# Performance work log

Measured on AMD Instinct MI355X. Metric: run time of the kernel, lower is better.

Reference implementation:

```python
import jax, jax.numpy as jnp
import numpy as np

N, E, B, T = 50000, 800000, 256, 50
IN_DIM, H, C1, C2, Q_DIM, LH = 128, 4, 32, 128, 32, 128
EPS = 1e-5


def setup_inputs() -> dict:
    key = jax.random.key(0)
    ks = jax.random.split(key, 24)
    g = 0.05
    inp = {
        'x': jax.random.normal(ks[0], (N, IN_DIM), jnp.float32),
        'edge_index': jax.random.randint(ks[1], (2, E), 0, N, jnp.int32),
        'batch': jnp.sort(jax.random.randint(ks[2], (N,), 0, B, jnp.int32)),
        'quant': jax.random.normal(ks[3], (B, T, Q_DIM), jnp.float32),
        # GATConv(128 -> 32, heads=4, concat)
        'gat_W': jax.random.normal(ks[4], (IN_DIM, H * C1), jnp.float32) * g,
        'gat_att_src': jax.random.normal(ks[5], (H, C1), jnp.float32) * g,
        'gat_att_dst': jax.random.normal(ks[6], (H, C1), jnp.float32) * g,
        'gat_b': jnp.zeros((H * C1,), jnp.float32),
        # BN1 over 128 channels (eval mode)
        'bn1_gamma': jnp.ones((H * C1,), jnp.float32),
        'bn1_beta': jnp.zeros((H * C1,), jnp.float32),
        'bn1_mean': jax.random.normal(ks[7], (H * C1,), jnp.float32) * 0.01,
        'bn1_var': jnp.ones((H * C1,), jnp.float32),
        # GCNConv(128 -> 128)
        'gcn_W': jax.random.normal(ks[8], (H * C1, C2), jnp.float32) * g,
        'gcn_b': jnp.zeros((C2,), jnp.float32),
        'bn2_gamma': jnp.ones((C2,), jnp.float32),
        'bn2_beta': jnp.zeros((C2,), jnp.float32),
        'bn2_mean': jax.random.normal(ks[9], (C2,), jnp.float32) * 0.01,
        'bn2_var': jnp.ones((C2,), jnp.float32),
        # GlobalAttention gate: Linear(C2 -> 1)
        'gate_W': jax.random.normal(ks[10], (1, C2), jnp.float32) * g,
        'gate_b': jnp.zeros((1,), jnp.float32),
        # LSTM(Q_DIM -> LH), torch gate order i,f,g,o
        'lstm_Wih': jax.random.normal(ks[11], (4 * LH, Q_DIM), jnp.float32) * g,
        'lstm_Whh': jax.random.normal(ks[12], (4 * LH, LH), jnp.float32) * g,
        'lstm_bih': jnp.zeros((4 * LH,), jnp.float32),
        'lstm_bhh': jnp.zeros((4 * LH,), jnp.float32),
        # final Linear(C2+LH -> 1)
        'fc_W': jax.random.normal(ks[13], (1, C2 + LH), jnp.float32) * g,
        'fc_b': jnp.zeros((1,), jnp.float32),
    }
    return inp


def _segment_softmax(e, seg, num_segments):
    m = jax.ops.segment_max(e, seg, num_segments=num_segments)
    ex = jnp.exp(e - m[seg])
    s = jax.ops.segment_sum(ex, seg, num_segments=num_segments)
    return ex / (s[seg] + 1e-16)


def _bn_eval(x, gamma, beta, mean, var):
    return gamma * (x - mean) * jax.lax.rsqrt(var + EPS) + beta


def _forward(x, edge_index, batch, quant,
             gat_W, gat_att_src, gat_att_dst, gat_b,
             bn1_gamma, bn1_beta, bn1_mean, bn1_var,
             gcn_W, gcn_b, bn2_gamma, bn2_beta, bn2_mean, bn2_var,
             gate_W, gate_b,
             lstm_Wih, lstm_Whh, lstm_bih, lstm_bhh,
             fc_W, fc_b):
    n = x.shape[0]
    loops = jnp.arange(n, dtype=edge_index.dtype)
    ei = jnp.concatenate([edge_index, jnp.stack([loops, loops])], axis=1)  # add self loops
    src, dst = ei[0], ei[1]

    # ---- GATConv ----
    xw = (x @ gat_W).reshape(n, H, C1)                      # [N,H,C1]
    a_src = jnp.sum(xw * gat_att_src, axis=-1)              # [N,H]
    a_dst = jnp.sum(xw * gat_att_dst, axis=-1)
    e = jax.nn.leaky_relu(a_src[src] + a_dst[dst], 0.2)     # [E+N,H]
    alpha = _segment_softmax(e, dst, n)                     # softmax over in-edges per dst
    msg = xw[src] * alpha[:, :, None]                       # [E+N,H,C1]
    h = jax.ops.segment_sum(msg, dst, num_segments=n).reshape(n, H * C1) + gat_b

    h = jax.nn.elu(h)
    h = _bn_eval(h, bn1_gamma, bn1_beta, bn1_mean, bn1_var)

    # ---- GCNConv (sym-normalized with self loops) ----
    deg = jax.ops.segment_sum(jnp.ones_like(dst, jnp.float32), dst, num_segments=n)
    dinv = jnp.where(deg > 0, jax.lax.rsqrt(deg), 0.0)
    norm = dinv[src] * dinv[dst]                            # [E+N]
    hw = h @ gcn_W                                          # [N,C2]
    h2 = jax.ops.segment_sum(hw[src] * norm[:, None], dst, num_segments=n) + gcn_b

    h2 = jax.nn.elu(h2)
    h2 = _bn_eval(h2, bn2_gamma, bn2_beta, bn2_mean, bn2_var)

    # ---- GlobalAttention pooling over graphs ----
    gate = (h2 @ gate_W.T + gate_b)[:, 0]                   # [N]
    score = _segment_softmax(gate, batch, B)
    graph_rep = jax.ops.segment_sum(score[:, None] * h2, batch, num_segments=B)  # [B,C2]

    # ---- LSTM over quant series ----
    def step(carry, xt):
        hh, cc = carry
        gates = xt @ lstm_Wih.T + hh @ lstm_Whh.T + lstm_bih + lstm_bhh
        i, f, gg, o = jnp.split(gates, 4, axis=-1)
        cc = jax.nn.sigmoid(f) * cc + jax.nn.sigmoid(i) * jnp.tanh(gg)
        hh = jax.nn.sigmoid(o) * jnp.tanh(cc)
        return (hh, cc), None

    h0 = jnp.zeros((B, LH), quant.dtype)
    (hT, _), _ = jax.lax.scan(step, (h0, h0), jnp.swapaxes(quant, 0, 1))

    combined = jnp.concatenate([graph_rep, hT], axis=1)     # [B, C2+LH]
    out = (combined @ fc_W.T + fc_b)[:, 0]                  # [B]
    return out


def reference(x, edge_index, batch, quant,
              gat_W, gat_att_src, gat_att_dst, gat_b,
              bn1_gamma, bn1_beta, bn1_mean, bn1_var,
              gcn_W, gcn_b, bn2_gamma, bn2_beta, bn2_mean, bn2_var,
              gate_W, gate_b,
              lstm_Wih, lstm_Whh, lstm_bih, lstm_bhh,
              fc_W, fc_b):
    return _forward(x, edge_index, batch, quant,
                    gat_W, gat_att_src, gat_att_dst, gat_b,
                    bn1_gamma, bn1_beta, bn1_mean, bn1_var,
                    gcn_W, gcn_b, bn2_gamma, bn2_beta, bn2_mean, bn2_var,
                    gate_W, gate_b,
                    lstm_Wih, lstm_Whh, lstm_bih, lstm_bhh,
                    fc_W, fc_b)
```

## Files before the change

kernel.cpp:

```cpp
#include <hip/hip_runtime.h>
#include <cfloat>
#include <cstddef>

constexpr int KIN   = 128;
constexpr int KQD   = 32;
constexpr int KT    = 50;
constexpr int KLH   = 128;
constexpr float BN_EPS = 1e-5f;

typedef __attribute__((ext_vector_type(8))) short bf16x8;
typedef __attribute__((ext_vector_type(4))) float f32x4;
union U8 { bf16x8 v; unsigned u[4]; };

__device__ __forceinline__ float elu_f(float x)  { return x > 0.f ? x : (__expf(x) - 1.f); }
__device__ __forceinline__ float leaky_f(float x){ return x > 0.f ? x : 0.2f * x; }

__device__ __forceinline__ unsigned bfpack(float lo, float hi) {
    unsigned ul = __float_as_uint(lo), uh = __float_as_uint(hi);
    ul += 0x7FFFu + ((ul >> 16) & 1u);
    uh += 0x7FFFu + ((uh >> 16) & 1u);
    return (ul >> 16) | (uh & 0xFFFF0000u);
}
__device__ __forceinline__ unsigned short bf1(float v) {
    unsigned u = __float_as_uint(v);
    u += 0x7FFFu + ((u >> 16) & 1u);
    return (unsigned short)(u >> 16);
}
__device__ __forceinline__ float bflo(unsigned u) { return __uint_as_float(u << 16); }
__device__ __forceinline__ float bfhi(unsigned u) { return __uint_as_float(u & 0xFFFF0000u); }

__device__ __forceinline__ bf16x8 pack8(float4 p, float4 q) {
    U8 t;
    t.u[0] = bfpack(p.x, p.y); t.u[1] = bfpack(p.z, p.w);
    t.u[2] = bfpack(q.x, q.y); t.u[3] = bfpack(q.z, q.w);
    return t.v;
}

__global__ void k_deg(const int* __restrict__ ei, int E, int* __restrict__ deg) {
    int e = blockIdx.x * blockDim.x + threadIdx.x;
    if (e < E) atomicAdd(&deg[ei[E + e]], 1);
}

__global__ __launch_bounds__(1024)
void k_scan_a(const int* __restrict__ deg, int n, int* __restrict__ bsum) {
    __shared__ int wsum[16];
    int tid = threadIdx.x, lane = tid & 63, w = tid >> 6;
    int i0 = blockIdx.x * 4096 + tid * 4;
    int t = 0;
    #pragma unroll
    for (int j = 0; j < 4; j++) t += (i0 + j < n) ? deg[i0 + j] : 0;
    #pragma unroll
    for (int d = 1; d < 64; d <<= 1) t += __shfl_xor(t, d);
    if (lane == 0) wsum[w] = t;
    __syncthreads();
    if (tid == 0) {
        int s = 0;
        #pragma unroll
        for (int k = 0; k < 16; k++) s += wsum[k];
        bsum[blockIdx.x] = s;
    }
}

__global__ void k_scan_b(int* __restrict__ bsum, int nb) {
    if (threadIdx.x == 0) {
        int run = 0;
        for (int i = 0; i < nb; i++) { int v = bsum[i]; bsum[i] = run; run += v; }
    }
}

__global__ __launch_bounds__(1024)
void k_scan_c(const int* __restrict__ deg, int n, const int* __restrict__ bsum,
              int* __restrict__ offsets, int* __restrict__ cursor,
              float* __restrict__ dinv) {
    __shared__ int wsum[16];
    int tid = threadIdx.x, lane = tid & 63, w = tid >> 6;
    int i0 = blockIdx.x * 4096 + tid * 4;
    int v[4];
    #pragma unroll
    for (int j = 0; j < 4; j++) v[j] = (i0 + j < n) ? deg[i0 + j] : 0;
    int tsum = v[0] + v[1] + v[2] + v[3];
    int sc = tsum;
    #pragma unroll
    for (int d = 1; d < 64; d <<= 1) {
        int o = __shfl_up(sc, d);
        if (lane >= d) sc += o;
    }
    if (lane == 63) wsum[w] = sc;
    __syncthreads();
    if (w == 0) {
        int xx = (lane < 16) ? wsum[lane] : 0;
        #pragma unroll
        for (int d = 1; d < 16; d <<= 1) {
            int o = __shfl_up(xx, d);
            if (lane >= d) xx += o;
        }
        if (lane < 16) wsum[lane] = xx;
    }
    __syncthreads();
    int run = bsum[blockIdx.x] + ((w > 0) ? wsum[w - 1] : 0) + sc - tsum;
    #pragma unroll
    for (int j = 0; j < 4; j++) {
        int i = i0 + j;
        if (i < n) {
            cursor[i]      = run;
            offsets[i + 1] = run + v[j];
            dinv[i]        = rsqrtf((float)(v[j] + 1));
            run += v[j];
        }
    }
    if (blockIdx.x == 0 && tid == 0) offsets[0] = 0;
}

template <bool ATT>
__global__ __launch_bounds__(256, 4)
void k_gemm_mfma(const float* __restrict__ X, const float* __restrict__ W,
                 unsigned* __restrict__ Yb, int nrows,
                 const float* __restrict__ attS, const float* __restrict__ attD,
                 float* __restrict__ a_src, float* __restrict__ a_dst) {
    __shared__ float tile[16][132];
    __shared__ float as_sh[128], ad_sh[128];
    int tid  = threadIdx.x;
    int lane = tid & 63;
    int wv   = tid >> 6;
    if (ATT && tid < 128) { as_sh[tid] = attS[tid]; ad_sh[tid] = attD[tid]; }
    int l16 = lane & 15;
    int kq  = (lane >> 4) * 8;
    bf16x8 bfr[2][4];
    #pragma unroll
    for (int nt = 0; nt < 2; nt++) {
        int n = wv * 32 + nt * 16 + l16;
        #pragma unroll
        for (int kk = 0; kk < 4; kk++) {
            int k0 = kk * 32 + kq;
            float f[8];
            #pragma unroll
            for (int j = 0; j < 8; j++) f[j] = W[(size_t)(k0 + j) * 128 + n];
            U8 t;
            t.u[0] = bfpack(f[0], f[1]); t.u[1] = bfpack(f[2], f[3]);
            t.u[2] = bfpack(f[4], f[5]); t.u[3] = bfpack(f[6], f[7]);
            bfr[nt][kk] = t.v;
        }
    }
    int nch = (nrows + 15) / 16;
    for (int ch = blockIdx.x; ch < nch; ch += gridDim.x) {
        int r0 = ch * 16;
        int r  = r0 + l16;
        bool rok = r < nrows;
        const float* xr = X + (size_t)r * 128 + kq;
        float4 z4 = make_float4(0.f, 0.f, 0.f, 0.f);
        bf16x8 afr[4];
        #pragma unroll
        for (int kk = 0; kk < 4; kk++) {
            float4 p = rok ? *reinterpret_cast<const float4*>(xr + kk * 32)     : z4;
            float4 q = rok ? *reinterpret_cast<const float4*>(xr + kk * 32 + 4) : z4;
            afr[kk] = pack8(p, q);
        }
        f32x4 acc0 = {0.f, 0.f, 0.f, 0.f};
        f32x4 acc1 = {0.f, 0.f, 0.f, 0.f};
        #pragma unroll
        for (int kk = 0; kk < 4; kk++) {
            acc0 = __builtin_amdgcn_mfma_f32_16x16x32_bf16(afr[kk], bfr[0][kk], acc0, 0, 0, 0);
            acc1 = __builtin_amdgcn_mfma_f32_16x16x32_bf16(afr[kk], bfr[1][kk], acc1, 0, 0, 0);
        }
        __syncthreads();
        int rowb = (lane >> 4) * 4;
        int cb   = wv * 32 + l16;
        #pragma unroll
        for (int reg = 0; reg < 4; reg++) {
            tile[rowb + reg][cb]      = acc0[reg];
            tile[rowb + reg][cb + 16] = acc1[reg];
        }
        __syncthreads();
        #pragma unroll
        for (int i = 0; i < 4; i++) {
            int idx = tid + i * 256;
            int row = idx >> 6, cp = idx & 63;
            int rr = r0 + row;
            if (rr < nrows) {
                float2 f = *reinterpret_cast<const float2*>(&tile[row][cp * 2]);
                Yb[(size_t)rr * 64 + cp] = bfpack(f.x, f.y);
            }
        }
        if (ATT && tid < 64) {
            int rr2 = tid >> 2, h = tid & 3;
            if (r0 + rr2 < nrows) {
                float ps = 0.f, pd = 0.f;
                #pragma unroll
                for (int j = 0; j < 32; j++) {
                    float v = tile[rr2][h * 32 + j];
                    ps += v * as_sh[h * 32 + j];
                    pd += v * ad_sh[h * 32 + j];
                }
                a_src[(size_t)(r0 + rr2) * 4 + h] = ps;
                a_dst[(size_t)(r0 + rr2) * 4 + h] = pd;
            }
        }
    }
}

__global__ __launch_bounds__(256)
void k_gat_agg(const int* __restrict__ offsets, const int* __restrict__ csr_src,
               const float* __restrict__ a_src, const float* __restrict__ a_dst,
               const unsigned* __restrict__ xwb, const float* __restrict__ bias,
               const float* __restrict__ g1, const float* __restrict__ b1,
               const float* __restrict__ mu1, const float* __restrict__ var1,
               float* __restrict__ hout, int n) {
    __shared__ int   src_sh[4][64];
    __shared__ float al_sh[4][4][64];
    int lane = threadIdx.x & 63;
    int wv   = threadIdx.x >> 6;
    int wid  = (blockIdx.x * blockDim.x + threadIdx.x) >> 6;
    int nw   = (gridDim.x * blockDim.x) >> 6;
    int hP   = lane >> 4;
    int c0 = lane * 2, c1 = c0 + 1;
    float bi0 = bias[c0], bi1 = bias[c1];
    float A0 = g1[c0] * rsqrtf(var1[c0] + BN_EPS);
    float A1 = g1[c1] * rsqrtf(var1[c1] + BN_EPS);
    float B0 = b1[c0] - mu1[c0] * A0;
    float B1 = b1[c1] - mu1[c1] * A1;
    for (int node = wid; node < n; node += nw) {
        int beg = offsets[node], end = offsets[node + 1];
        int rowlen = end - beg, total = rowlen + 1;
        float4 adv = *reinterpret_cast<const float4*>(&a_dst[(size_t)node * 4]);
        int sv = (lane < rowlen) ? csr_src[beg + lane] : node;
        float4 as4 = *reinterpret_cast<const float4*>(&a_src[(size_t)sv * 4]);
        float e0 = leaky_f(as4.x + adv.x), e1 = leaky_f(as4.y + adv.y);
        float e2 = leaky_f(as4.z + adv.z), e3 = leaky_f(as4.w + adv.w);
        float m[4] = {-FLT_MAX, -FLT_MAX, -FLT_MAX, -FLT_MAX};
        if (lane < total) { m[0] = e0; m[1] = e1; m[2] = e2; m[3] = e3; }
        for (int i = lane + 64; i < total; i += 64) {
            int src = (i < rowlen) ? csr_src[beg + i] : node;
            float4 a4 = *reinterpret_cast<const float4*>(&a_src[(size_t)src * 4]);
            m[0] = fmaxf(m[0], leaky_f(a4.x + adv.x));
            m[1] = fmaxf(m[1], leaky_f(a4.y + adv.y));
            m[2] = fmaxf(m[2], leaky_f(a4.z + adv.z));
            m[3] = fmaxf(m[3], leaky_f(a4.w + adv.w));
        }
        #pragma unroll
        for (int off = 32; off; off >>= 1) {
            #pragma unroll
            for (int h = 0; h < 4; h++) m[h] = fmaxf(m[h], __shfl_xor(m[h], off));
        }
        float ex[4] = {0.f, 0.f, 0.f, 0.f};
        if (lane < total) {
            ex[0] = __expf(e0 - m[0]); ex[1] = __expf(e1 - m[1]);
            ex[2] = __expf(e2 - m[2]); ex[3] = __expf(e3 - m[3]);
        }
        float s[4] = {ex[0], ex[1], ex[2], ex[3]};
        for (int i = lane + 64; i < total; i += 64) {
            int src = (i < rowlen) ? csr_src[beg + i] : node;
            float4 a4 = *reinterpret_cast<const float4*>(&a_src[(size_t)src * 4]);
            s[0] += __expf(leaky_f(a4.x + adv.x) - m[0]);
            s[1] += __expf(leaky_f(a4.y + adv.y) - m[1]);
            s[2] += __expf(leaky_f(a4.z + adv.z) - m[2]);
            s[3] += __expf(leaky_f(a4.w + adv.w) - m[3]);
        }
        #pragma unroll
        for (int off = 32; off; off >>= 1) {
            #pragma unroll
            for (int h = 0; h < 4; h++) s[h] += __shfl_xor(s[h], off);
        }
        float inv[4];
        #pragma unroll
        for (int h = 0; h < 4; h++) inv[h] = 1.f / (s[h] + 1e-16f);
        src_sh[wv][lane] = sv;
        #pragma unroll
        for (int h = 0; h < 4; h++) al_sh[wv][h][lane] = ex[h] * inv[h];
        __builtin_amdgcn_wave_barrier();
        float acc0 = 0.f, acc1 = 0.f;
        int cnt = min(total, 64);
        {
            int i = 0;
            for (; i + 8 <= cnt; i += 8) {
                int   sj[8]; float aj[8]; unsigned uj[8];
                #pragma unroll
                for (int q = 0; q < 8; q++) { sj[q] = src_sh[wv][i + q]; aj[q] = al_sh[wv][hP][i + q]; }
                #pragma unroll
                for (int q = 0; q < 8; q++) uj[q] = xwb[(size_t)sj[q] * 64 + lane];
                #pragma unroll
                for (int q = 0; q < 8; q++) { acc0 += aj[q] * bflo(uj[q]); acc1 += aj[q] * bfhi(uj[q]); }
            }
            for (; i < cnt; i++) {
                int src  = src_sh[wv][i];
                float aP = al_sh[wv][hP][i];
                unsigned u = xwb[(size_t)src * 64 + lane];
                acc0 += aP * bflo(u);
                acc1 += aP * bfhi(u);
            }
        }
        for (int base = 64; base < total; base += 64) {
            __builtin_amdgcn_wave_barrier();
            int i = base + lane;
            int src2 = node;
            float a0v = 0.f, a1v = 0.f, a2v = 0.f, a3v = 0.f;
            if (i < total) {
                if (i < rowlen) src2 = csr_src[beg + i];
                float4 a4 = *reinterpret_cast<const float4*>(&a_src[(size_t)src2 * 4]);
                a0v = __expf(leaky_f(a4.x + adv.x) - m[0]) * inv[0];
                a1v = __expf(leaky_f(a4.y + adv.y) - m[1]) * inv[1];
                a2v = __expf(leaky_f(a4.z + adv.z) - m[2]) * inv[2];
                a3v = __expf(leaky_f(a4.w + adv.w) - m[3]) * inv[3];
            }
            src_sh[wv][lane] = src2;
            al_sh[wv][0][lane] = a0v; al_sh[wv][1][lane] = a1v;
            al_sh[wv][2][lane] = a2v; al_sh[wv][3][lane] = a3v;
            __builtin_amdgcn_wave_barrier();
            int cnt2 = min(total - base, 64);
            for (int j = 0; j < cnt2; j++) {
                int src  = src_sh[wv][j];
                float aP = al_sh[wv][hP][j];
                unsigned u = xwb[(size_t)src * 64 + lane];
                acc0 += aP * bflo(u);
                acc1 += aP * bfhi(u);
            }
        }
        __builtin_amdgcn_wave_barrier();
        float vA = elu_f(acc0 + bi0);
        float vB = elu_f(acc1 + bi1);
        vA = vA * A0 + B0;
        vB = vB * A1 + B1;
        *reinterpret_cast<float2*>(&hout[(size_t)node * 128 + c0]) =
            make_float2(vA, vB);
    }
}

__global__ __launch_bounds__(256)
void k_gcn_agg(const int* __restrict__ offsets, const int* __restrict__ csr_src,
               const float* __restrict__ dinv, const unsigned* __restrict__ hwb,
               const float* __restrict__ bias,
               const float* __restrict__ g2, const float* __restrict__ b2,
               const float* __restrict__ mu2, const float* __restrict__ var2,
               const float* __restrict__ gateW, const float* __restrict__ gateB,
               float* __restrict__ h2, float* __restrict__ gate, int n) {
    __shared__ int   src_sh[4][64];
    __shared__ float w_sh[4][64];
    int lane = threadIdx.x & 63;
    int wv   = threadIdx.x >> 6;
    int wid  = (blockIdx.x * blockDim.x + threadIdx.x) >> 6;
    int nw   = (gridDim.x * blockDim.x) >> 6;
    int c0 = lane * 2, c1 = c0 + 1;
    float bi0 = bias[c0], bi1 = bias[c1];
    float A0 = g2[c0] * rsqrtf(var2[c0] + BN_EPS);
    float A1 = g2[c1] * rsqrtf(var2[c1] + BN_EPS);
    float B0 = b2[c0] - mu2[c0] * A0;
    float B1 = b2[c1] - mu2[c1] * A1;
    float gw0 = gateW[c0], gw1 = gateW[c1], gB = gateB[0];
    for (int node = wid; node < n; node += nw) {
        int beg = offsets[node], end = offsets[node + 1];
        int rowlen = end - beg;
        float dn = dinv[node];
        unsigned us = hwb[(size_t)node * 64 + lane];
        float acc0 = dn * dn * bflo(us);
        float acc1 = dn * dn * bfhi(us);
        for (int base = 0; base < rowlen; base += 64) {
            __builtin_amdgcn_wave_barrier();
            int i = base + lane;
            int src2 = node;
            float wv2 = 0.f;
            if (i < rowlen) { src2 = csr_src[beg + i]; wv2 = dinv[src2] * dn; }
            src_sh[wv][lane] = src2;
            w_sh[wv][lane]   = wv2;
            __builtin_amdgcn_wave_barrier();
            int cnt = min(rowlen - base, 64);
            int j = 0;
            for (; j + 8 <= cnt; j += 8) {
                int   sj[8]; float wj[8]; unsigned uj[8];
                #pragma unroll
                for (int q = 0; q < 8; q++) { sj[q] = src_sh[wv][j + q]; wj[q] = w_sh[wv][j + q]; }
                #pragma unroll
                for (int q = 0; q < 8; q++) uj[q] = hwb[(size_t)sj[q] * 64 + lane];
                #pragma unroll
                for (int q = 0; q < 8; q++) { acc0 += wj[q] * bflo(uj[q]); acc1 += wj[q] * bfhi(uj[q]); }
            }
            for (; j < cnt; j++) {
                int src = src_sh[wv][j];
                float w = w_sh[wv][j];
                unsigned u = hwb[(size_t)src * 64 + lane];
                acc0 += w * bflo(u);
                acc1 += w * bfhi(u);
            }
        }
        __builtin_amdgcn_wave_barrier();
        float vA = elu_f(acc0 + bi0);
        float vB = elu_f(acc1 + bi1);
        vA = vA * A0 + B0;
        vB = vB * A1 + B1;
        *reinterpret_cast<float2*>(&h2[(size_t)node * 128 + c0]) =
            make_float2(vA, vB);
        float p = vA * gw0 + vB * gw1;
        #pragma unroll
        for (int off = 32; off; off >>= 1) p += __shfl_xor(p, off);
        if (lane == 0) gate[node] = p + gB;
    }
}

__device__ __forceinline__ int lbound(const int* a, int n, int key) {
    int lo = 0, hi = n;
    while (lo < hi) { int mid = (lo + hi) >> 1; if (a[mid] < key) lo = mid + 1; else hi = mid; }
    return lo;
}

__global__ __launch_bounds__(256)
void k_pool(const int* __restrict__ batch, const float* __restrict__ gate,
            const float* __restrict__ h2, const float* __restrict__ hT,
            const float* __restrict__ fcW, const float* __restrict__ fcB,
            float* __restrict__ out, int n) {
    int b = blockIdx.x, tid = threadIdx.x;
    __shared__ float red[256];
    __shared__ float sc_sh[256];
    int start = lbound(batch, n, b);
    int end   = lbound(batch, n, b + 1);
    float m = -FLT_MAX;
    for (int i = start + tid; i < end; i += 256) m = fmaxf(m, gate[i]);
    red[tid] = m; __syncthreads();
    for (int s2 = 128; s2 > 0; s2 >>= 1) {
        if (tid < s2) red[tid] = fmaxf(red[tid], red[tid + s2]);
        __syncthreads();
    }
    m = red[0]; __syncthreads();
    float s = 0.f;
    for (int i = start + tid; i < end; i += 256) s += __expf(gate[i] - m);
    red[tid] = s; __syncthreads();
    for (int s2 = 128; s2 > 0; s2 >>= 1) {
        if (tid < s2) red[tid] += red[tid + s2];
        __syncthreads();
    }
    float inv = 1.f / (red[0] + 1e-16f);
    __syncthreads();
    int j = tid & 127, half = tid >> 7;
    float acc = 0.f;
    for (int base = start; base < end; base += 256) {
        int cnt = min(256, end - base);
        __syncthreads();
        if (tid < cnt) sc_sh[tid] = __expf(gate[base + tid] - m) * inv;
        __syncthreads();
        for (int ii = half; ii < cnt; ii += 2)
            acc += sc_sh[ii] * h2[(size_t)(base + ii) * 128 + j];
    }
    red[tid] = acc; __syncthreads();
    if (half == 0) sc_sh[j] = red[j] + red[128 + j];
    __syncthreads();
    float p = 0.f;
    if (tid < 128)
        p = fcW[tid] * sc_sh[tid] + fcW[128 + tid] * hT[(size_t)b * 128 + tid];
    red[tid] = p; __syncthreads();
    for (int s2 = 128; s2 > 0; s2 >>= 1) {
        if (tid < s2) red[tid] += red[tid + s2];
        __syncthreads();
    }
    if (tid == 0) out[b] = red[0] + fcB[0];
}

__global__ __launch_bounds__(256)
void k_xproj(const float* __restrict__ quant, const float* __restrict__ Wih,
             const float* __restrict__ bih, const float* __restrict__ bhh,
             float* __restrict__ xproj) {
    int blk = blockIdx.x;
    int chunk = blk / KT, s = blk % KT;
    int lane = threadIdx.x & 63, w = threadIdx.x >> 6;
    int l15 = lane & 15, kq8 = (lane >> 4) * 8;
    int b = chunk * 16 + l15;
    const float* xr = &quant[(size_t)b * (KT * KQD) + s * KQD + kq8];
    bf16x8 ax = pack8(*reinterpret_cast<const float4*>(xr),
                      *reinterpret_cast<const float4*>(xr + 4));
    #pragma unroll
    for (int ti = 0; ti < 8; ti++) {
        int tc = w * 8 + ti;
        int gcol = w * 128 + ti * 16 + l15;
        const float* wr = &Wih[(size_t)gcol * KQD + kq8];
        bf16x8 bw = pack8(*reinterpret_cast<const float4*>(wr),
                          *reinterpret_cast<const float4*>(wr + 4));
        f32x4 acc = {0.f, 0.f, 0.f, 0.f};
        acc = __builtin_amdgcn_mfma_f32_16x16x32_bf16(ax, bw, acc, 0, 0, 0);
        float bv = bih[gcol] + bhh[gcol];
        acc[0] += bv; acc[1] += bv; acc[2] += bv; acc[3] += bv;
        *reinterpret_cast<f32x4*>(
            &xproj[(((size_t)chunk * KT + s) * 32 + tc) * 256 + lane * 4]) = acc;
    }
}

struct GemmSh { float tile[16][132]; float as[128]; float ad[128]; };
struct LstmSh { unsigned short h16[2][16][148]; };
union  FusedSh { GemmSh g; LstmSh l; };

__global__ __launch_bounds__(512)
void k_fused(
             const float* __restrict__ xproj, const float* __restrict__ Whh,
             float* __restrict__ hstate, int nchunks,
             const float* __restrict__ X, const float* __restrict__ W,
             unsigned* __restrict__ Yb, int nrows,
             const float* __restrict__ attS, const float* __restrict__ attD,
             float* __restrict__ a_src, float* __restrict__ a_dst, int ngemm,
             const int* __restrict__ ei, int E, int* __restrict__ cursor,
             int* __restrict__ csr_src) {
    __shared__ FusedSh sh;
    int bid = (int)blockIdx.x;
    int t = threadIdx.x, lane = t & 63, w = t >> 6;

    if (bid >= nchunks + ngemm) {
        int e = (bid - nchunks - ngemm) * 512 + t;
        if (e < E) {
            int s = ei[e], d = ei[E + e];
            int pos = atomicAdd(&cursor[d], 1);
            csr_src[pos] = s;
        }
        return;
    }

    int l15 = lane & 15, kq8 = (lane >> 4) * 8;

    if (bid >= nchunks) {
        if (t < 128) { sh.g.as[t] = attS[t]; sh.g.ad[t] = attD[t]; }
        int n = w * 16 + l15;
        bf16x8 bfr[4];
        #pragma unroll
        for (int kk = 0; kk < 4; kk++) {
            int k0 = kk * 32 + kq8;
            float f[8];
            #pragma unroll
            for (int jj = 0; jj < 8; jj++) f[jj] = W[(size_t)(k0 + jj) * 128 + n];
            U8 tp;
            tp.u[0] = bfpack(f[0], f[1]); tp.u[1] = bfpack(f[2], f[3]);
            tp.u[2] = bfpack(f[4], f[5]); tp.u[3] = bfpack(f[6], f[7]);
            bfr[kk] = tp.v;
        }
        int nch = (nrows + 15) / 16;
        for (int ch = bid - nchunks; ch < nch; ch += ngemm) {
            int r0 = ch * 16;
            int r  = r0 + l15;
            bool rok = r < nrows;
            const float* xr = X + (size_t)r * 128 + kq8;
            float4 z4 = make_float4(0.f, 0.f, 0.f, 0.f);
            bf16x8 afr[4];
            #pragma unroll
            for (int kk = 0; kk < 4; kk++) {
                float4 p = rok ? *reinterpret_cast<const float4*>(xr + kk * 32)     : z4;
                float4 q = rok ? *reinterpret_cast<const float4*>(xr + kk * 32 + 4) : z4;
                afr[kk] = pack8(p, q);
            }
            f32x4 acc = {0.f, 0.f, 0.f, 0.f};
            #pragma unroll
            for (int kk = 0; kk < 4; kk++)
                acc = __builtin_amdgcn_mfma_f32_16x16x32_bf16(afr[kk], bfr[kk], acc, 0, 0, 0);
            __syncthreads();
            int rowb = (lane >> 4) * 4;
            #pragma unroll
            for (int reg = 0; reg < 4; reg++)
                sh.g.tile[rowb + reg][n] = acc[reg];
            __syncthreads();
            #pragma unroll
            for (int i = 0; i < 2; i++) {
                int idx = t + i * 512;
                int row = idx >> 6, cp = idx & 63;
                int rr = r0 + row;
                if (rr < nrows) {
                    float2 f = *reinterpret_cast<const float2*>(&sh.g.tile[row][cp * 2]);
                    Yb[(size_t)rr * 64 + cp] = bfpack(f.x, f.y);
                }
            }
            if (t < 64) {
                int rr2 = t >> 2, h = t & 3;
                if (r0 + rr2 < nrows) {
                    float ps = 0.f, pd = 0.f;
                    #pragma unroll
                    for (int jj = 0; jj < 32; jj++) {
                        float v = sh.g.tile[rr2][h * 32 + jj];
                        ps += v * sh.g.as[h * 32 + jj];
                        pd += v * sh.g.ad[h * 32 + jj];
                    }
                    a_src[(size_t)(r0 + rr2) * 4 + h] = ps;
                    a_dst[(size_t)(r0 + rr2) * 4 + h] = pd;
                }
            }
        }
        return;
    }

    int chunk = bid;
    int j = w * 16 + l15;
    int rowq = (lane >> 4) * 4;
    bf16x8 whh_f[4][4];
    #pragma unroll
    for (int c = 0; c < 4; c++) {
        int col = c * 128 + j;
        #pragma unroll
        for (int kk = 0; kk < 4; kk++) {
            const float* wr = &Whh[(size_t)col * 128 + kk * 32 + kq8];
            whh_f[c][kk] = pack8(*reinterpret_cast<const float4*>(wr),
                                 *reinterpret_cast<const float4*>(wr + 4));
        }
    }
    for (int p = t; p < 16 * 148; p += 512) {
        int r = p / 148, cc = p - r * 148;
        sh.l.h16[0][r][cc] = 0;
    }
    float cst[4] = {0.f, 0.f, 0.f, 0.f};
    const float* xb = xproj + ((size_t)chunk * KT) * 32 * 256;
    f32x4 xgA = *reinterpret_cast<const f32x4*>(&xb[(0 * 8 + w) * 256 + lane * 4]);
    f32x4 xgB = *reinterpret_cast<const f32x4*>(&xb[(1 * 8 + w) * 256 + lane * 4]);
    f32x4 xgC = *reinterpret_cast<const f32x4*>(&xb[(2 * 8 + w) * 256 + lane * 4]);
    f32x4 xgD = *reinterpret_cast<const f32x4*>(&xb[(3 * 8 + w) * 256 + lane * 4]);
    int cur = 0;
    __syncthreads();
    for (int s = 0; s < KT; s++) {
        f32x4 nA, nB, nC, nD;
        if (s + 1 < KT) {
            const float* xs = &xb[((size_t)(s + 1) * 32 + w) * 256 + lane * 4];
            nA = *reinterpret_cast<const f32x4*>(&xs[0 * 8 * 256]);
            nB = *reinterpret_cast<const f32x4*>(&xs[1 * 8 * 256]);
            nC = *reinterpret_cast<const f32x4*>(&xs[2 * 8 * 256]);
            nD = *reinterpret_cast<const f32x4*>(&xs[3 * 8 * 256]);
        }
        f32x4 ai = xgA, af = xgB, ag = xgC, ao = xgD;
        #pragma unroll
        for (int kk = 0; kk < 4; kk++) {
            bf16x8 ah = *reinterpret_cast<const bf16x8*>(&sh.l.h16[cur][l15][kk * 32 + kq8]);
            ai = __builtin_amdgcn_mfma_f32_16x16x32_bf16(ah, whh_f[0][kk], ai, 0, 0, 0);
            af = __builtin_amdgcn_mfma_f32_16x16x32_bf16(ah, whh_f[1][kk], af, 0, 0, 0);
            ag = __builtin_amdgcn_mfma_f32_16x16x32_bf16(ah, whh_f[2][kk], ag, 0, 0, 0);
            ao = __builtin_amdgcn_mfma_f32_16x16x32_bf16(ah, whh_f[3][kk], ao, 0, 0, 0);
        }
        int nxt = cur ^ 1;
        #pragma unroll
        for (int r = 0; r < 4; r++) {
            float eiv = __expf(fminf(-ai[r], 25.f));
            float efv = __expf(fminf(-af[r], 25.f));
            float egv = __expf(fminf(2.f * ag[r], 50.f));
            float eov = __expf(fminf(-ao[r], 25.f));
            float pi = 1.f + eiv, pf = 1.f + efv;
            float gp = egv + 1.f, gm = egv - 1.f;
            float P  = pi * gp;
            float D  = pf * P;
            float cn = fmaf(cst[r], P, gm * pf) * __builtin_amdgcn_rcpf(D);
            cst[r] = cn;
            float ecv = __expf(fminf(2.f * cn, 50.f));
            float D2  = (1.f + eov) * (ecv + 1.f);
            float hv  = (ecv - 1.f) * __builtin_amdgcn_rcpf(D2);
            sh.l.h16[nxt][rowq + r][j] = bf1(hv);
        }
        xgA = nA; xgB = nB; xgC = nC; xgD = nD;
        __syncthreads();
        cur = nxt;
    }
    int b0 = chunk * 16;
    for (int p = t; p < 16 * KLH; p += 512) {
        int row = p >> 7, jj = p & 127;
        hstate[(size_t)(b0 + row) * KLH + jj] =
            __uint_as_float((unsigned)sh.l.h16[cur][row][jj] << 16);
    }
}

extern "C" void kernel_launch(void* const* d_in, const int* in_sizes, int n_in,
                              void* d_out, int out_size, void* d_ws, size_t ws_size,
                              hipStream_t stream) {
    const float* x     = (const float*)d_in[0];
    const int*   ei    = (const int*)  d_in[1];
    const int*   batch = (const int*)  d_in[2];
    const float* quant = (const float*)d_in[3];
    const float* gatW  = (const float*)d_in[4];
    const float* attS  = (const float*)d_in[5];
    const float* attD  = (const float*)d_in[6];
    const float* gatB  = (const float*)d_in[7];
    const float* bn1g  = (const float*)d_in[8];
    const float* bn1b  = (const float*)d_in[9];
    const float* bn1m  = (const float*)d_in[10];
    const float* bn1v  = (const float*)d_in[11];
    const float* gcnW  = (const float*)d_in[12];
    const float* gcnB  = (const float*)d_in[13];
    const float* bn2g  = (const float*)d_in[14];
    const float* bn2b  = (const float*)d_in[15];
    const float* bn2m  = (const float*)d_in[16];
    const float* bn2v  = (const float*)d_in[17];
    const float* gateW = (const float*)d_in[18];
    const float* gateB = (const float*)d_in[19];
    const float* Wih   = (const float*)d_in[20];
    const float* Whh   = (const float*)d_in[21];
    const float* bih   = (const float*)d_in[22];
    const float* bhh   = (const float*)d_in[23];
    const float* fcW   = (const float*)d_in[24];
    const float* fcB   = (const float*)d_in[25];

    int N = in_sizes[0] / KIN;
    int E = in_sizes[1] / 2;
    int B = in_sizes[3] / (KT * KQD);
    int nchunks = B / 16;

    char* ws = (char*)d_ws;
    size_t off = 0;
    auto alloc = [&](size_t bytes) -> void* {
        void* p = ws + off;
        off += (bytes + 511) & ~(size_t)511;
        return p;
    };
    int nb = (N + 4095) / 4096;
    int*      deg     = (int*)     alloc((size_t)N * 4);
    int*      offsets = (int*)     alloc((size_t)(N + 1) * 4);
    int*      cursor  = (int*)     alloc((size_t)N * 4);
    float*    dinv    = (float*)   alloc((size_t)N * 4);
    int*      csr_src = (int*)     alloc((size_t)E * 4);
    int*      bsum    = (int*)     alloc((size_t)nb * 4);
    float*    a_src   = (float*)   alloc((size_t)N * 16);
    float*    a_dst   = (float*)   alloc((size_t)N * 16);
    unsigned* xwb     = (unsigned*)alloc((size_t)N * 256);
    float*    hbuf    = (float*)   alloc((size_t)N * 512);
    float*    gate    = (float*)   alloc((size_t)N * 4);
    float*    hstate  = (float*)   alloc((size_t)B * KLH * 4);
    float*    xproj   = (float*)   alloc((size_t)nchunks * KT * 32 * 256 * 4);

    hipMemsetAsync(deg, 0, (size_t)N * 4, stream);
    int eb = (E + 255) / 256;
    k_deg   <<<eb, 256, 0, stream>>>(ei, E, deg);
    k_scan_a<<<nb, 1024, 0, stream>>>(deg, N, bsum);
    k_scan_b<<<1, 64, 0, stream>>>(bsum, nb);
    k_scan_c<<<nb, 1024, 0, stream>>>(deg, N, bsum, offsets, cursor, dinv);

    k_xproj<<<nchunks * KT, 256, 0, stream>>>(quant, Wih, bih, bhh, xproj);

    int ngemm = 1024;
    int nfill = (E + 511) / 512;
    k_fused<<<nchunks + ngemm + nfill, 512, 0, stream>>>(
        xproj, Whh, hstate, nchunks,
        x, gatW, xwb, N, attS, attD, a_src, a_dst, ngemm,
        ei, E, cursor, csr_src);

    k_gat_agg<<<3072, 256, 0, stream>>>(offsets, csr_src, a_src, a_dst, xwb, gatB,
                                        bn1g, bn1b, bn1m, bn1v, hbuf, N);
    k_gemm_mfma<false><<<1024, 256, 0, stream>>>(hbuf, gcnW, xwb, N,
                                                 nullptr, nullptr, nullptr, nullptr);
    k_gcn_agg<<<3072, 256, 0, stream>>>(offsets, csr_src, dinv, xwb, gcnB,
                                        bn2g, bn2b, bn2m, bn2v, gateW, gateB,
                                        hbuf, gate, N);
    k_pool<<<B, 256, 0, stream>>>(batch, gate, hbuf, hstate, fcW, fcB,
                                  (float*)d_out, N);
}
```

Measured before the change: 385.3 us.

## Pre-bin edges by destination bucket before CSR fill; raise LSTM wave priority

Adds a two-pass binning stage. Edges are first grouped into 128-node destination buckets through per-block shared-memory histograms and staging, and written as (src,dst) pairs. Each fill block in the fused kernel then scatters one bucket, so cursor atomics and csr_src writes fall in a small local address range instead of random positions across the whole array. The LSTM chunk blocks also set a higher wave priority during the recurrence so the serial critical path competes better with the co-resident GEMM and fill blocks. The cost is an extra pass over the edges and an 8-byte-per-edge intermediate buffer, plus two more kernel launches.

```diff
diff --git a/kernel.cpp b/kernel.cpp
--- a/kernel.cpp
+++ b/kernel.cpp
@@ -7,6 +7,7 @@
 constexpr int KT    = 50;
 constexpr int KLH   = 128;
 constexpr float BN_EPS = 1e-5f;
+constexpr int NBK   = 512;
 
 typedef __attribute__((ext_vector_type(8))) short bf16x8;
 typedef __attribute__((ext_vector_type(4))) float f32x4;
@@ -109,6 +110,69 @@
         }
     }
     if (blockIdx.x == 0 && tid == 0) offsets[0] = 0;
+}
+
+__global__ void k_binit(const int* __restrict__ offsets, int* __restrict__ bcur,
+                        int nbuck, int n) {
+    int b = blockIdx.x * blockDim.x + threadIdx.x;
+    if (b < nbuck) bcur[b] = offsets[min(b << 7, n)];
+}
+
+__global__ __launch_bounds__(256)
+void k_bin1(const int* __restrict__ ei, int E, int* __restrict__ bcur,
+            uint2* __restrict__ binpairs) {
+    __shared__ int   hist[NBK];
+    __shared__ int   pref[NBK];
+    __shared__ int   lcur[NBK];
+    __shared__ int   gbase[NBK];
+    __shared__ int   wsum[4];
+    __shared__ uint2 stage[4096];
+    int t = threadIdx.x, lane = t & 63, w = t >> 6;
+    for (int base = blockIdx.x * 4096; base < E; base += gridDim.x * 4096) {
+        int cnt = min(4096, E - base);
+        for (int i = t; i < NBK; i += 256) hist[i] = 0;
+        __syncthreads();
+        for (int i = t; i < cnt; i += 256) {
+            int d = ei[E + base + i];
+            atomicAdd(&hist[d >> 7], 1);
+        }
+        __syncthreads();
+        int v0 = hist[2 * t], v1 = hist[2 * t + 1];
+        int tsum = v0 + v1;
+        int sc = tsum;
+        #pragma unroll
+        for (int d = 1; d < 64; d <<= 1) {
+            int o = __shfl_up(sc, d);
+            if (lane >= d) sc += o;
+        }
+        if (lane == 63) wsum[w] = sc;
+        __syncthreads();
+        int woff = 0;
+        for (int k = 0; k < w; k++) woff += wsum[k];
+        int excl = woff + sc - tsum;
+        pref[2 * t]     = excl;
+        pref[2 * t + 1] = excl + v0;
+        lcur[2 * t]     = excl;
+        lcur[2 * t + 1] = excl + v0;
+        __syncthreads();
+        for (int i = t; i < cnt; i += 256) {
+            int s = ei[base + i], d = ei[E + base + i];
+            int pos = atomicAdd(&lcur[d >> 7], 1);
+            stage[pos] = make_uint2((unsigned)s, (unsigned)d);
+        }
+        __syncthreads();
+        for (int b = t; b < NBK; b += 256) {
+            int c = hist[b];
+            gbase[b] = c ? atomicAdd(&bcur[b], c) : 0;
+        }
+        __syncthreads();
+        for (int i = t; i < cnt; i += 256) {
+            uint2 p = stage[i];
+            int b = (int)(p.y >> 7);
+            binpairs[gbase[b] + (i - pref[b])] = p;
+        }
+        __syncthreads();
+    }
 }
 
 template <bool ATT>
@@ -491,18 +555,22 @@
              unsigned* __restrict__ Yb, int nrows,
              const float* __restrict__ attS, const float* __restrict__ attD,
              float* __restrict__ a_src, float* __restrict__ a_dst, int ngemm,
-             const int* __restrict__ ei, int E, int* __restrict__ cursor,
-             int* __restrict__ csr_src) {
+             const uint2* __restrict__ binpairs, const int* __restrict__ offsets,
+             int* __restrict__ cursor, int* __restrict__ csr_src, int nbuck, int N) {
     __shared__ FusedSh sh;
     int bid = (int)blockIdx.x;
     int t = threadIdx.x, lane = t & 63, w = t >> 6;
 
     if (bid >= nchunks + ngemm) {
-        int e = (bid - nchunks - ngemm) * 512 + t;
-        if (e < E) {
-            int s = ei[e], d = ei[E + e];
-            int pos = atomicAdd(&cursor[d], 1);
-            csr_src[pos] = s;
+        int b = bid - nchunks - ngemm;
+        if (b < nbuck) {
+            int rb = offsets[min(b << 7, N)];
+            int re = offsets[min((b + 1) << 7, N)];
+            for (int i = rb + t; i < re; i += 512) {
+                uint2 p = binpairs[i];
+                int pos = atomicAdd(&cursor[p.y], 1);
+                csr_src[pos] = (int)p.x;
+            }
         }
         return;
     }
@@ -576,6 +644,7 @@
         return;
     }
 
+    __builtin_amdgcn_s_setprio(1);
     int chunk = bid;
     int j = w * 16 + l15;
     int rowq = (lane >> 4) * 4;
@@ -642,6 +711,7 @@
         __syncthreads();
         cur = nxt;
     }
+    __builtin_amdgcn_s_setprio(0);
     int b0 = chunk * 16;
     for (int p = t; p < 16 * KLH; p += 512) {
         int row = p >> 7, jj = p & 127;
@@ -684,6 +754,7 @@
     int E = in_sizes[1] / 2;
     int B = in_sizes[3] / (KT * KQD);
     int nchunks = B / 16;
+    int nbuck = (N + 127) >> 7;
 
     char* ws = (char*)d_ws;
     size_t off = 0;
@@ -693,19 +764,21 @@
         return p;
     };
     int nb = (N + 4095) / 4096;
-    int*      deg     = (int*)     alloc((size_t)N * 4);
-    int*      offsets = (int*)     alloc((size_t)(N + 1) * 4);
-    int*      cursor  = (int*)     alloc((size_t)N * 4);
-    float*    dinv    = (float*)   alloc((size_t)N * 4);
-    int*      csr_src = (int*)     alloc((size_t)E * 4);
-    int*      bsum    = (int*)     alloc((size_t)nb * 4);
-    float*    a_src   = (float*)   alloc((size_t)N * 16);
-    float*    a_dst   = (float*)   alloc((size_t)N * 16);
-    unsigned* xwb     = (unsigned*)alloc((size_t)N * 256);
-    float*    hbuf    = (float*)   alloc((size_t)N * 512);
-    float*    gate    = (float*)   alloc((size_t)N * 4);
-    float*    hstate  = (float*)   alloc((size_t)B * KLH * 4);
-    float*    xproj   = (float*)   alloc((size_t)nchunks * KT * 32 * 256 * 4);
+    int*      deg      = (int*)     alloc((size_t)N * 4);
+    int*      offsets  = (int*)     alloc((size_t)(N + 1) * 4);
+    int*      cursor   = (int*)     alloc((size_t)N * 4);
+    float*    dinv     = (float*)   alloc((size_t)N * 4);
+    int*      csr_src  = (int*)     alloc((size_t)E * 4);
+    int*      bsum     = (int*)     alloc((size_t)nb * 4);
+    int*      bcur     = (int*)     alloc((size_t)NBK * 4);
+    uint2*    binpairs = (uint2*)   alloc((size_t)E * 8);
+    float*    a_src    = (float*)   alloc((size_t)N * 16);
+    float*    a_dst    = (float*)   alloc((size_t)N * 16);
+    unsigned* xwb      = (unsigned*)alloc((size_t)N * 256);
+    float*    hbuf     = (float*)   alloc((size_t)N * 512);
+    float*    gate     = (float*)   alloc((size_t)N * 4);
+    float*    hstate   = (float*)   alloc((size_t)B * KLH * 4);
+    float*    xproj    = (float*)   alloc((size_t)nchunks * KT * 32 * 256 * 4);
 
     hipMemsetAsync(deg, 0, (size_t)N * 4, stream);
     int eb = (E + 255) / 256;
@@ -713,15 +786,16 @@
     k_scan_a<<<nb, 1024, 0, stream>>>(deg, N, bsum);
     k_scan_b<<<1, 64, 0, stream>>>(bsum, nb);
     k_scan_c<<<nb, 1024, 0, stream>>>(deg, N, bsum, offsets, cursor, dinv);
+    k_binit <<<(nbuck + 255) / 256, 256, 0, stream>>>(offsets, bcur, nbuck, N);
+    k_bin1  <<<256, 256, 0, stream>>>(ei, E, bcur, binpairs);
 
     k_xproj<<<nchunks * KT, 256, 0, stream>>>(quant, Wih, bih, bhh, xproj);
 
     int ngemm = 1024;
-    int nfill = (E + 511) / 512;
-    k_fused<<<nchunks + ngemm + nfill, 512, 0, stream>>>(
+    k_fused<<<nchunks + ngemm + nbuck, 512, 0, stream>>>(
         xproj, Whh, hstate, nchunks,
         x, gatW, xwb, N, attS, attD, a_src, a_dst, ngemm,
-        ei, E, cursor, csr_src);
+        binpairs, offsets, cursor, csr_src, nbuck, N);
 
     k_gat_agg<<<3072, 256, 0, stream>>>(offsets, csr_src, a_src, a_dst, xwb, gatB,
                                         bn1g, bn1b, bn1m, bn1v, hbuf, N);
```

New measurement: 390.9 us (median of 4 runs). Within noise of the previous version (+1.5%).
